# Kernel tuning notes

Hardware: AMD Instinct MI355X
Metric: run time of the kernel (lower is better)

The kernel has to match this reference:

```python
import jax, jax.numpy as jnp
import numpy as np

# pywt 'db2' filter bank (decomposition and reconstruction), float32
DEC_LO = jnp.array([-0.12940952255092145, 0.22414386804185735, 0.836516303737469, 0.48296291314469025], dtype=jnp.float32)
DEC_HI = jnp.array([-0.48296291314469025, 0.836516303737469, -0.22414386804185735, -0.12940952255092145], dtype=jnp.float32)
REC_LO = jnp.array([0.48296291314469025, 0.836516303737469, 0.22414386804185735, -0.12940952255092145], dtype=jnp.float32)
REC_HI = jnp.array([-0.12940952255092145, -0.22414386804185735, 0.836516303737469, -0.48296291314469025], dtype=jnp.float32)
_FLEN = 4
_DN = ('NCW', 'OIW', 'NCW')


def _convolve(x, f, stride, padding, lhs_dilation=1):
    # np.convolve-style convolution (kernel flipped) along last axis; x: (B, n)
    k = f[::-1][None, None, :]
    y = jax.lax.conv_general_dilated(x[:, None, :], k, (stride,), padding,
                                     lhs_dilation=(lhs_dilation,),
                                     dimension_numbers=_DN)
    return y[:, 0, :]


def _dwt_db2(x):
    # pywt.dwt(x, 'db2', mode='symmetric') along last axis; n even.
    # symmetric extension by flen-1=3 on each side, valid convolution, take odd indices.
    ext = jnp.concatenate([x[:, 2::-1], x, x[:, -1:-4:-1]], axis=1)[:, 1:]
    cA = _convolve(ext, DEC_LO, 2, 'VALID')  # (B, n/2+1)
    cD = _convolve(ext, DEC_HI, 2, 'VALID')
    return cA, cD


def _idwt_db2(cA, cD):
    # pywt.idwt(cA, cD, 'db2'): upsample-by-2 convolution with rec filters,
    # trimmed to length 2L - flen + 2. Equivalent to lhs_dilation=2, pad (1,1).
    lo = _convolve(cA, REC_LO, 1, [(1, 1)], lhs_dilation=2)
    hi = _convolve(cD, REC_HI, 1, [(1, 1)], lhs_dilation=2)
    return lo + hi  # (B, n)


def setup_inputs() -> dict:
    key = jax.random.key(0)
    k1, k2 = jax.random.split(key)
    B, D = 65536, 512
    x = jax.random.normal(k1, (B, D), dtype=jnp.float32)
    weight = jax.random.normal(k2, (2, D // 2 + 1), dtype=jnp.float32)
    return {"x": x, "weight": weight}


def reference(x, weight):
    shape = x.shape
    x2 = x.reshape(-1, shape[-1])
    cA, cD = _dwt_db2(x2)
    z = _idwt_db2(cA, weight[0] * cD)
    return jax.nn.leaky_relu(z.reshape(shape), negative_slope=0.01)
```

## Files before the change

kernel.cpp:

```cpp
#include <hip/hip_runtime.h>
#include <stdint.h>


#define N     512
#define NC    257
#define ROWS  2
#define CPAD  260

__global__ __launch_bounds__(256) void wavelet_kernel(
    const float* __restrict__ x,
    const float* __restrict__ w,
    float* __restrict__ out)
{
    constexpr float DL0 = -0.12940952255092145f, DL1 = 0.22414386804185735f,
                    DL2 =  0.836516303737469f,   DL3 = 0.48296291314469025f;
    constexpr float DH0 = -0.48296291314469025f, DH1 = 0.836516303737469f,
                    DH2 = -0.22414386804185735f, DH3 = -0.12940952255092145f;
    constexpr float RL0 =  0.48296291314469025f, RL1 = 0.836516303737469f,
                    RL2 =  0.22414386804185735f, RL3 = -0.12940952255092145f;
    constexpr float RH0 = -0.12940952255092145f, RH1 = -0.22414386804185735f,
                    RH2 =  0.836516303737469f,   RH3 = -0.48296291314469025f;

    __shared__ float xs[ROWS][N];
    __shared__ float sA[ROWS][CPAD];
    __shared__ float sD[ROWS][CPAD];
    __shared__ float wf[NC];

    const int tid = threadIdx.x;
    const size_t base = (size_t)blockIdx.x * (ROWS * N);

    wf[tid] = w[tid];
    if (tid == 0) wf[256] = w[256];

    {
        float4 v = ((const float4*)(x + base))[tid];
        int e = tid << 2;
        int r = e >> 9;
        int c = e & (N - 1);
        *(float4*)&xs[r][c] = v;
    }
    __syncthreads();

    #pragma unroll
    for (int r = 0; r < ROWS; ++r) {
        {
            int i = tid;
            float v0, v1, v2, v3;
            if (i == 0) {
                v0 = xs[r][1]; v1 = xs[r][0]; v2 = xs[r][0]; v3 = xs[r][1];
            } else {
                int b = 2 * i - 2;
                v0 = xs[r][b]; v1 = xs[r][b + 1]; v2 = xs[r][b + 2]; v3 = xs[r][b + 3];
            }
            float a = DL3 * v0 + DL2 * v1 + DL1 * v2 + DL0 * v3;
            float d = DH3 * v0 + DH2 * v1 + DH1 * v2 + DH0 * v3;
            sA[r][i] = a;
            sD[r][i] = d * wf[i];
        }
        if (tid == 0) {
            float v0 = xs[r][510], v1 = xs[r][511], v2 = xs[r][511], v3 = xs[r][510];
            float a = DL3 * v0 + DL2 * v1 + DL1 * v2 + DL0 * v3;
            float d = DH3 * v0 + DH2 * v1 + DH1 * v2 + DH0 * v3;
            sA[r][256] = a;
            sD[r][256] = d * wf[256];
        }
    }
    __syncthreads();

    {
        int e  = tid << 2;
        int r  = e >> 9;
        int c  = e & (N - 1);
        int ib = c >> 1;
        float A0 = sA[r][ib],     D0 = sD[r][ib];
        float A1 = sA[r][ib + 1], D1 = sD[r][ib + 1];
        float A2 = sA[r][ib + 2], D2 = sD[r][ib + 2];

        float z0 = RL2 * A0 + RL0 * A1 + RH2 * D0 + RH0 * D1;
        float z1 = RL3 * A0 + RL1 * A1 + RH3 * D0 + RH1 * D1;
        float z2 = RL2 * A1 + RL0 * A2 + RH2 * D1 + RH0 * D2;
        float z3 = RL3 * A1 + RL1 * A2 + RH3 * D1 + RH1 * D2;

        float4 o;
        o.x = z0 >= 0.f ? z0 : 0.01f * z0;
        o.y = z1 >= 0.f ? z1 : 0.01f * z1;
        o.z = z2 >= 0.f ? z2 : 0.01f * z2;
        o.w = z3 >= 0.f ? z3 : 0.01f * z3;
        ((float4*)(out + base))[tid] = o;
    }
}

extern "C" void kernel_launch(void* const* d_in, const int* in_sizes, int n_in,
                              void* d_out, int out_size, void* d_ws, size_t ws_size,
                              hipStream_t stream) {
    const float* x = (const float*)d_in[0];
    const float* w = (const float*)d_in[1];
    float* out = (float*)d_out;

    int rows   = in_sizes[0] / N;
    int blocks = rows / ROWS;
    wavelet_kernel<<<blocks, 256, 0, stream>>>(x, w, out);
}
```

Baseline: 223.9 us.

## Fuse DWT and IDWT per thread using neighbor exchange through shared memory

Each thread now computes its own three approximation/detail coefficients straight from its float4 plus two neighbor values taken from a transposed shared buffer. This removes the sA/sD staging, the second barrier and the redundant coefficient work. Loads and stores also switch to nontemporal builtins to avoid polluting the cache on streaming data. Coefficients at tile boundaries are now computed redundantly by adjacent threads, a small extra ALU cost.

After: 223.9 us. No clear change (-0.0%).

```diff
diff --git a/kernel.cpp b/kernel.cpp
--- a/kernel.cpp
+++ b/kernel.cpp
@@ -2,10 +2,10 @@
 #include <stdint.h>
 
 
-#define N     512
-#define NC    257
-#define ROWS  2
-#define CPAD  260
+#define N   512
+#define NC  257
+
+typedef float f4v __attribute__((ext_vector_type(4)));
 
 __global__ __launch_bounds__(256) void wavelet_kernel(
     const float* __restrict__ x,
@@ -21,73 +21,55 @@
     constexpr float RH0 = -0.12940952255092145f, RH1 = -0.22414386804185735f,
                     RH2 =  0.836516303737469f,   RH3 = -0.48296291314469025f;
 
-    __shared__ float xs[ROWS][N];
-    __shared__ float sA[ROWS][CPAD];
-    __shared__ float sD[ROWS][CPAD];
+    __shared__ float xt[4][256];
     __shared__ float wf[NC];
 
     const int tid = threadIdx.x;
-    const size_t base = (size_t)blockIdx.x * (ROWS * N);
+    const size_t base = (size_t)blockIdx.x * 1024;
 
     wf[tid] = w[tid];
     if (tid == 0) wf[256] = w[256];
 
-    {
-        float4 v = ((const float4*)(x + base))[tid];
-        int e = tid << 2;
-        int r = e >> 9;
-        int c = e & (N - 1);
-        *(float4*)&xs[r][c] = v;
-    }
+    f4v v = __builtin_nontemporal_load(((const f4v*)(x + base)) + tid);
+    xt[0][tid] = v.x;
+    xt[1][tid] = v.y;
+    xt[2][tid] = v.z;
+    xt[3][tid] = v.w;
     __syncthreads();
 
-    #pragma unroll
-    for (int r = 0; r < ROWS; ++r) {
-        {
-            int i = tid;
-            float v0, v1, v2, v3;
-            if (i == 0) {
-                v0 = xs[r][1]; v1 = xs[r][0]; v2 = xs[r][0]; v3 = xs[r][1];
-            } else {
-                int b = 2 * i - 2;
-                v0 = xs[r][b]; v1 = xs[r][b + 1]; v2 = xs[r][b + 2]; v3 = xs[r][b + 3];
-            }
-            float a = DL3 * v0 + DL2 * v1 + DL1 * v2 + DL0 * v3;
-            float d = DH3 * v0 + DH2 * v1 + DH1 * v2 + DH0 * v3;
-            sA[r][i] = a;
-            sD[r][i] = d * wf[i];
-        }
-        if (tid == 0) {
-            float v0 = xs[r][510], v1 = xs[r][511], v2 = xs[r][511], v3 = xs[r][510];
-            float a = DL3 * v0 + DL2 * v1 + DL1 * v2 + DL0 * v3;
-            float d = DH3 * v0 + DH2 * v1 + DH1 * v2 + DH0 * v3;
-            sA[r][256] = a;
-            sD[r][256] = d * wf[256];
-        }
-    }
-    __syncthreads();
+    const int col = (tid << 2) & (N - 1);
+    const int lm = (tid == 0)   ? 0   : tid - 1;
+    const int lp = (tid == 255) ? 255 : tid + 1;
 
-    {
-        int e  = tid << 2;
-        int r  = e >> 9;
-        int c  = e & (N - 1);
-        int ib = c >> 1;
-        float A0 = sA[r][ib],     D0 = sD[r][ib];
-        float A1 = sA[r][ib + 1], D1 = sD[r][ib + 1];
-        float A2 = sA[r][ib + 2], D2 = sD[r][ib + 2];
+    float xl0 = xt[2][lm], xl1 = xt[3][lm];
+    float xr0 = xt[0][lp], xr1 = xt[1][lp];
 
-        float z0 = RL2 * A0 + RL0 * A1 + RH2 * D0 + RH0 * D1;
-        float z1 = RL3 * A0 + RL1 * A1 + RH3 * D0 + RH1 * D1;
-        float z2 = RL2 * A1 + RL0 * A2 + RH2 * D1 + RH0 * D2;
-        float z3 = RL3 * A1 + RL1 * A2 + RH3 * D1 + RH1 * D2;
+    if (col == 0)     { xl0 = v.y; xl1 = v.x; }
+    if (col == N - 4) { xr0 = v.w; xr1 = v.z; }
 
-        float4 o;
-        o.x = z0 >= 0.f ? z0 : 0.01f * z0;
-        o.y = z1 >= 0.f ? z1 : 0.01f * z1;
-        o.z = z2 >= 0.f ? z2 : 0.01f * z2;
-        o.w = z3 >= 0.f ? z3 : 0.01f * z3;
-        ((float4*)(out + base))[tid] = o;
-    }
+    float A0 = DL3 * xl0 + DL2 * xl1 + DL1 * v.x + DL0 * v.y;
+    float D0 = DH3 * xl0 + DH2 * xl1 + DH1 * v.x + DH0 * v.y;
+    float A1 = DL3 * v.x + DL2 * v.y + DL1 * v.z + DL0 * v.w;
+    float D1 = DH3 * v.x + DH2 * v.y + DH1 * v.z + DH0 * v.w;
+    float A2 = DL3 * v.z + DL2 * v.w + DL1 * xr0 + DL0 * xr1;
+    float D2 = DH3 * v.z + DH2 * v.w + DH1 * xr0 + DH0 * xr1;
+
+    const int i0 = col >> 1;
+    D0 *= wf[i0];
+    D1 *= wf[i0 + 1];
+    D2 *= wf[i0 + 2];
+
+    float z0 = RL2 * A0 + RL0 * A1 + RH2 * D0 + RH0 * D1;
+    float z1 = RL3 * A0 + RL1 * A1 + RH3 * D0 + RH1 * D1;
+    float z2 = RL2 * A1 + RL0 * A2 + RH2 * D1 + RH0 * D2;
+    float z3 = RL3 * A1 + RL1 * A2 + RH3 * D1 + RH1 * D2;
+
+    f4v o;
+    o.x = z0 >= 0.f ? z0 : 0.01f * z0;
+    o.y = z1 >= 0.f ? z1 : 0.01f * z1;
+    o.z = z2 >= 0.f ? z2 : 0.01f * z2;
+    o.w = z3 >= 0.f ? z3 : 0.01f * z3;
+    __builtin_nontemporal_store(o, ((f4v*)(out + base)) + tid);
 }
 
 extern "C" void kernel_launch(void* const* d_in, const int* in_sizes, int n_in,
@@ -97,7 +79,6 @@
     const float* w = (const float*)d_in[1];
     float* out = (float*)d_out;
 
-    int rows   = in_sizes[0] / N;
-    int blocks = rows / ROWS;
+    int blocks = in_sizes[0] / 1024;
     wavelet_kernel<<<blocks, 256, 0, stream>>>(x, w, out);
 }
```
